# Performance work log

Measured on AMD Instinct MI355X. Metric: run time of the kernel, lower is better.

## Reference

```python
import jax, jax.numpy as jnp
import numpy as np

N_NODES = 100000
E_ORIG = 600000   # entries in edge_dict_original -> nodes of second stage
E_LINE = 1200000  # edges among edge-nodes
H = 128
OUT = 64
BN_EPS = 1e-5
N_LAYERS = 2  # num_initial_gin_layers == num_gin_layers == 2


def setup_inputs() -> dict:
    key = jax.random.key(0)
    ks = iter(jax.random.split(key, 64))
    def nrm(shape, s=0.05):
        return jax.random.normal(next(ks), shape, jnp.float32) * s
    inp = {}
    inp["edge_index"] = jax.random.randint(next(ks), (2, E_LINE), 0, E_ORIG)
    inp["x_original"] = jax.random.normal(next(ks), (N_NODES, H), jnp.float32)
    inp["edge_index_original"] = jax.random.randint(next(ks), (2, E_ORIG), 0, N_NODES)
    inp["edge_pairs"] = jax.random.randint(next(ks), (E_ORIG, 2), 0, N_NODES)
    for pfx in ("init", "gin"):
        inp[pfx + "_W1"] = nrm((N_LAYERS, H, H))
        inp[pfx + "_b1"] = nrm((N_LAYERS, H))
        inp[pfx + "_g"] = jnp.ones((N_LAYERS, H), jnp.float32) + nrm((N_LAYERS, H))
        inp[pfx + "_bb"] = nrm((N_LAYERS, H))
        inp[pfx + "_m"] = nrm((N_LAYERS, H))
        inp[pfx + "_v"] = jnp.ones((N_LAYERS, H), jnp.float32) + jax.random.uniform(next(ks), (N_LAYERS, H), jnp.float32) * 0.1
        inp[pfx + "_W2"] = nrm((N_LAYERS, H, H))
        inp[pfx + "_b2"] = nrm((N_LAYERS, H))
    inp["mlp_W1"] = nrm((H, H)); inp["mlp_b1"] = nrm((H,))
    inp["mlp_g"] = jnp.ones((H,), jnp.float32) + nrm((H,))
    inp["mlp_bb"] = nrm((H,)); inp["mlp_m"] = nrm((H,))
    inp["mlp_v"] = jnp.ones((H,), jnp.float32) + jax.random.uniform(next(ks), (H,), jnp.float32) * 0.1
    inp["mlp_W2"] = nrm((H, H)); inp["mlp_b2"] = nrm((H,))
    inp["out_W"] = nrm((H, OUT)); inp["out_b"] = nrm((OUT,))
    return inp


def _bn(h, g, b, m, v):  # eval-mode BatchNorm1d
    return (h - m) * jax.lax.rsqrt(v + BN_EPS) * g + b


def _gin_conv(x, ei, n, W1, b1, g, bb, m, v, W2, b2):
    # GINConv (eps=0): nn(x + sum_{j in N(i)} x_j)
    agg = jax.ops.segment_sum(x[ei[0]], ei[1], num_segments=n)
    h = x + agg
    h = jax.nn.relu(_bn(h @ W1 + b1, g, bb, m, v))
    return jax.nn.relu(h @ W2 + b2)


def reference(edge_index, x_original, edge_index_original, edge_pairs,
              init_W1, init_b1, init_g, init_bb, init_m, init_v, init_W2, init_b2,
              mlp_W1, mlp_b1, mlp_g, mlp_bb, mlp_m, mlp_v, mlp_W2, mlp_b2,
              gin_W1, gin_b1, gin_g, gin_bb, gin_m, gin_v, gin_W2, gin_b2,
              out_W, out_b):
    x = x_original
    for i in range(N_LAYERS):  # initial GIN layers on original graph (dropout=eval identity)
        x = _gin_conv(x, edge_index_original, N_NODES,
                      init_W1[i], init_b1[i], init_g[i], init_bb[i], init_m[i], init_v[i],
                      init_W2[i], init_b2[i])
    # per-edge gather of node pairs; concat-then-split == two gathers
    def mlp(h):  # PyG MLP, 2 layers, plain last
        h = jax.nn.relu(_bn(h @ mlp_W1 + mlp_b1, mlp_g, mlp_bb, mlp_m, mlp_v))
        return h @ mlp_W2 + mlp_b2
    h = mlp(x[edge_pairs[:, 0]]) + mlp(x[edge_pairs[:, 1]])  # [E_ORIG, H]
    for i in range(N_LAYERS):  # GIN layers on edge-node graph
        h = _gin_conv(h, edge_index, E_ORIG,
                      gin_W1[i], gin_b1[i], gin_g[i], gin_bb[i], gin_m[i], gin_v[i],
                      gin_W2[i], gin_b2[i])
    return h @ out_W + out_b  # [E_ORIG, OUT]
```

## Files before the change

### kernel.cpp

```cpp
#include <hip/hip_runtime.h>
#include <hip/hip_bf16.h>

typedef __bf16 bf8_t __attribute__((ext_vector_type(8)));
typedef float  f32x4 __attribute__((ext_vector_type(4)));

constexpr int N_NODES = 100000;
constexpr int E_ORIG  = 600000;
constexpr int E_LINE  = 1200000;

static inline int cdiv(int a, int b) { return (a + b - 1) / b; }

enum { A_DENSE = 0, A_AGG = 1, A_PAIR = 2 };

__global__ void k_f2b(const float* __restrict__ X, __bf16* __restrict__ O, int n8) {
    int i = blockIdx.x * 256 + threadIdx.x;
    if (i >= n8) return;
    float4 a = ((const float4*)X)[2 * i], b = ((const float4*)X)[2 * i + 1];
    bf8_t o;
    o[0] = (__bf16)a.x; o[1] = (__bf16)a.y; o[2] = (__bf16)a.z; o[3] = (__bf16)a.w;
    o[4] = (__bf16)b.x; o[5] = (__bf16)b.y; o[6] = (__bf16)b.z; o[7] = (__bf16)b.w;
    ((bf8_t*)O)[i] = o;
}

__global__ void k_hist(const int* __restrict__ dst, int* __restrict__ cnt, int E) {
    int e = blockIdx.x * 256 + threadIdx.x;
    if (e < E) atomicAdd(&cnt[dst[e]], 1);
}

__global__ void k_scan1(const int* __restrict__ cnt, int* __restrict__ offs,
                        int* __restrict__ bsum, int n) {
    __shared__ int tmp[256];
    int i = blockIdx.x * 256 + threadIdx.x;
    int v = (i < n) ? cnt[i] : 0;
    tmp[threadIdx.x] = v; __syncthreads();
    #pragma unroll
    for (int d = 1; d < 256; d <<= 1) {
        int t = (threadIdx.x >= d) ? tmp[threadIdx.x - d] : 0;
        __syncthreads();
        tmp[threadIdx.x] += t;
        __syncthreads();
    }
    if (i < n) offs[i] = tmp[threadIdx.x] - v;
    if (threadIdx.x == 255) bsum[blockIdx.x] = tmp[255];
}

__global__ void k_scan2(int* __restrict__ bsum, int nb) {
    __shared__ int tmp[256];
    __shared__ int carry;
    if (threadIdx.x == 0) carry = 0;
    __syncthreads();
    for (int base = 0; base < nb; base += 256) {
        int i = base + threadIdx.x;
        int v = (i < nb) ? bsum[i] : 0;
        tmp[threadIdx.x] = v; __syncthreads();
        #pragma unroll
        for (int d = 1; d < 256; d <<= 1) {
            int t = (threadIdx.x >= d) ? tmp[threadIdx.x - d] : 0;
            __syncthreads();
            tmp[threadIdx.x] += t;
            __syncthreads();
        }
        int tot = tmp[255];
        if (i < nb) bsum[i] = tmp[threadIdx.x] - v + carry;
        __syncthreads();
        if (threadIdx.x == 0) carry += tot;
        __syncthreads();
    }
}

__global__ void k_scan3(int* __restrict__ offs, int* __restrict__ cur,
                        const int* __restrict__ bsum, int n) {
    int i = blockIdx.x * 256 + threadIdx.x;
    if (i >= n) return;
    int o = offs[i] + bsum[blockIdx.x];
    offs[i] = o;
    cur[i]  = o;
}

__global__ void k_fill(const int* __restrict__ src, const int* __restrict__ dst,
                       int* __restrict__ cur, int* __restrict__ adj, int E) {
    int e = blockIdx.x * 256 + threadIdx.x;
    if (e >= E) return;
    int p = atomicAdd(&cur[dst[e]], 1);
    adj[p] = src[e];
}

struct WPtrs { const float* p[10]; };

__global__ void k_packW(WPtrs wp, __bf16* __restrict__ out) {
    const float* W = wp.p[blockIdx.x];
    __bf16* O = out + (size_t)blockIdx.x * 16384;
    const float4* W4 = (const float4*)W;
    for (int e = threadIdx.x; e < 4096; e += 256) {
        float4 w = W4[e];
        unsigned flat = (unsigned)e * 4;
        unsigned k = flat >> 7, n = flat & 127;
        unsigned c = n >> 4, s = k >> 5, hi = (k >> 3) & 3, j = k & 7;
        unsigned l0 = (hi << 4) | (n & 15);
        unsigned base = ((c * 4 + s) * 64 + l0) * 8 + j;
        O[base]      = (__bf16)w.x;
        O[base + 8]  = (__bf16)w.y;
        O[base + 16] = (__bf16)w.z;
        O[base + 24] = (__bf16)w.w;
    }
}

template<int MODE, bool RELU2>
__launch_bounds__(256, 4)
__global__ void k_layer(const __bf16* __restrict__ X, int M,
                        const int* __restrict__ offs, const int* __restrict__ cnt,
                        const int* __restrict__ adj, const int* __restrict__ pairs,
                        const __bf16* __restrict__ Wp1, const __bf16* __restrict__ Wp2,
                        const float* __restrict__ b1,
                        const float* __restrict__ bg, const float* __restrict__ bb,
                        const float* __restrict__ bm, const float* __restrict__ bv,
                        const float* __restrict__ b2,
                        __bf16* __restrict__ out) {
    __shared__ __bf16 sA[128 * 128];

    const int tid  = threadIdx.x;
    const int lane = tid & 63;
    const int wv   = tid >> 6;
    const int rowBase = blockIdx.x * 128;
    const int m0 = lane & 15, kq = lane >> 4;

    if (MODE != A_DENSE) {
        const int c    = lane & 15;
        const int slot = lane >> 4;
        int sarr[8], narr[8];
        #pragma unroll
        for (int p = 0; p < 8; ++p) {
            int grow = rowBase + wv * 32 + p * 4 + slot;
            int g = grow < M ? grow : 0;
            sarr[p] = offs[g];
            narr[p] = grow < M ? cnt[g] : 0;
        }
        int pa0[8], pa1[8];
        #pragma unroll
        for (int p = 0; p < 8; ++p) {
            pa0[p] = narr[p] > 0 ? adj[sarr[p]]     : 0;
            pa1[p] = narr[p] > 1 ? adj[sarr[p] + 1] : 0;
        }

        if (MODE == A_AGG) {
            #pragma unroll
            for (int half = 0; half < 2; ++half) {
                bf8_t sv[4], n0[4], n1[4];
                #pragma unroll
                for (int q = 0; q < 4; ++q) {
                    int p = half * 4 + q;
                    int grow = rowBase + wv * 32 + p * 4 + slot;
                    int g = grow < M ? grow : 0;
                    sv[q] = *((const bf8_t*)(X + (size_t)g      * 128) + c);
                    n0[q] = *((const bf8_t*)(X + (size_t)pa0[p] * 128) + c);
                    n1[q] = *((const bf8_t*)(X + (size_t)pa1[p] * 128) + c);
                }
                #pragma unroll
                for (int q = 0; q < 4; ++q) {
                    int p = half * 4 + q;
                    int rl = wv * 32 + p * 4 + slot;
                    int n = narr[p];
                    float acc[8];
                    #pragma unroll
                    for (int j = 0; j < 8; ++j) {
                        float a = (float)sv[q][j];
                        if (n > 0) a += (float)n0[q][j];
                        if (n > 1) a += (float)n1[q][j];
                        acc[j] = a;
                    }
                    int s = sarr[p], k = 2;
                    for (; k + 2 <= n; k += 2) {
                        int a0 = adj[s + k], a1 = adj[s + k + 1];
                        bf8_t v0 = *((const bf8_t*)(X + (size_t)a0 * 128) + c);
                        bf8_t v1 = *((const bf8_t*)(X + (size_t)a1 * 128) + c);
                        #pragma unroll
                        for (int j = 0; j < 8; ++j) acc[j] += (float)v0[j] + (float)v1[j];
                    }
                    if (k < n) {
                        int a0 = adj[s + k];
                        bf8_t v0 = *((const bf8_t*)(X + (size_t)a0 * 128) + c);
                        #pragma unroll
                        for (int j = 0; j < 8; ++j) acc[j] += (float)v0[j];
                    }
                    bf8_t o;
                    #pragma unroll
                    for (int j = 0; j < 8; ++j) o[j] = (__bf16)acc[j];
                    *(bf8_t*)&sA[rl * 128 + ((c ^ (rl & 7)) << 3)] = o;
                }
            }
        } else {
            #pragma unroll
            for (int half = 0; half < 2; ++half) {
                int2 spr[4], pq0[4], pq1[4];
                #pragma unroll
                for (int q = 0; q < 4; ++q) {
                    int p = half * 4 + q;
                    int grow = rowBase + wv * 32 + p * 4 + slot;
                    int g = grow < M ? grow : 0;
                    spr[q] = ((const int2*)pairs)[g];
                    pq0[q] = ((const int2*)pairs)[pa0[p]];
                    pq1[q] = ((const int2*)pairs)[pa1[p]];
                }
                #pragma unroll
                for (int q = 0; q < 4; ++q) {
                    int p = half * 4 + q;
                    int rl = wv * 32 + p * 4 + slot;
                    int n = narr[p];
                    bf8_t s0 = *((const bf8_t*)(X + (size_t)spr[q].x * 128) + c);
                    bf8_t s1 = *((const bf8_t*)(X + (size_t)spr[q].y * 128) + c);
                    bf8_t u0 = *((const bf8_t*)(X + (size_t)pq0[q].x * 128) + c);
                    bf8_t u1 = *((const bf8_t*)(X + (size_t)pq0[q].y * 128) + c);
                    bf8_t u2 = *((const bf8_t*)(X + (size_t)pq1[q].x * 128) + c);
                    bf8_t u3 = *((const bf8_t*)(X + (size_t)pq1[q].y * 128) + c);
                    float acc[8];
                    #pragma unroll
                    for (int j = 0; j < 8; ++j) {
                        float a = (float)s0[j] + (float)s1[j];
                        if (n > 0) a += (float)u0[j] + (float)u1[j];
                        if (n > 1) a += (float)u2[j] + (float)u3[j];
                        acc[j] = a;
                    }
                    int s = sarr[p];
                    for (int k = 2; k < n; ++k) {
                        int a0 = adj[s + k];
                        int2 qq = ((const int2*)pairs)[a0];
                        bf8_t w0 = *((const bf8_t*)(X + (size_t)qq.x * 128) + c);
                        bf8_t w1 = *((const bf8_t*)(X + (size_t)qq.y * 128) + c);
                        #pragma unroll
                        for (int j = 0; j < 8; ++j) acc[j] += (float)w0[j] + (float)w1[j];
                    }
                    bf8_t o;
                    #pragma unroll
                    for (int j = 0; j < 8; ++j) o[j] = (__bf16)acc[j];
                    *(bf8_t*)&sA[rl * 128 + ((c ^ (rl & 7)) << 3)] = o;
                }
            }
        }
    }

    f32x4 acc[2][8];
    #pragma unroll
    for (int rt = 0; rt < 2; ++rt)
        #pragma unroll
        for (int ct = 0; ct < 8; ++ct) acc[rt][ct] = (f32x4){0.f, 0.f, 0.f, 0.f};

    #pragma unroll
    for (int s = 0; s < 4; ++s) {
        bf8_t fa[2];
        #pragma unroll
        for (int rt = 0; rt < 2; ++rt) {
            int rl = wv * 32 + rt * 16 + m0;
            if (MODE == A_DENSE) {
                int r = rowBase + rl;
                r = r < M ? r : M - 1;
                fa[rt] = *(const bf8_t*)(X + (size_t)r * 128 + s * 32 + kq * 8);
            } else {
                int chunk = s * 4 + kq;
                fa[rt] = *(const bf8_t*)&sA[rl * 128 + ((chunk ^ (rl & 7)) << 3)];
            }
        }
        #pragma unroll
        for (int ct = 0; ct < 8; ++ct) {
            bf8_t fw = *(const bf8_t*)(Wp1 + ((size_t)((ct * 4 + s) * 64 + lane)) * 8);
            #pragma unroll
            for (int rt = 0; rt < 2; ++rt)
                acc[rt][ct] = __builtin_amdgcn_mfma_f32_16x16x32_bf16(fa[rt], fw, acc[rt][ct], 0, 0, 0);
        }
    }

    float S1r[8], T1r[8], T2r[8];
    #pragma unroll
    for (int ct = 0; ct < 8; ++ct) {
        int col = ct * 16 + m0;
        float b = b1[col];
        float g = bg[col], be = bb[col], m_ = bm[col], v_ = bv[col];
        float S = g * rsqrtf(v_ + 1e-5f);
        S1r[ct] = S;
        T1r[ct] = b * S + (be - m_ * S);
        T2r[ct] = b2[col];
    }

    #pragma unroll
    for (int rt = 0; rt < 2; ++rt) {
        #pragma unroll
        for (int r = 0; r < 4; ++r) {
            int rl = wv * 32 + rt * 16 + kq * 4 + r;
            #pragma unroll
            for (int ct = 0; ct < 8; ++ct) {
                int col = ct * 16 + m0;
                float v = acc[rt][ct][r] * S1r[ct] + T1r[ct];
                v = fmaxf(v, 0.f);
                int chunk = col >> 3;
                sA[rl * 128 + ((chunk ^ (rl & 7)) << 3) + (col & 7)] = (__bf16)v;
            }
        }
    }

    f32x4 acc2[2][8];
    #pragma unroll
    for (int rt = 0; rt < 2; ++rt)
        #pragma unroll
        for (int ct = 0; ct < 8; ++ct) acc2[rt][ct] = (f32x4){0.f, 0.f, 0.f, 0.f};

    #pragma unroll
    for (int s = 0; s < 4; ++s) {
        bf8_t fa[2];
        #pragma unroll
        for (int rt = 0; rt < 2; ++rt) {
            int rl = wv * 32 + rt * 16 + m0;
            int chunk = s * 4 + kq;
            fa[rt] = *(const bf8_t*)&sA[rl * 128 + ((chunk ^ (rl & 7)) << 3)];
        }
        #pragma unroll
        for (int ct = 0; ct < 8; ++ct) {
            bf8_t fw = *(const bf8_t*)(Wp2 + ((size_t)((ct * 4 + s) * 64 + lane)) * 8);
            #pragma unroll
            for (int rt = 0; rt < 2; ++rt)
                acc2[rt][ct] = __builtin_amdgcn_mfma_f32_16x16x32_bf16(fa[rt], fw, acc2[rt][ct], 0, 0, 0);
        }
    }

    #pragma unroll
    for (int rt = 0; rt < 2; ++rt) {
        #pragma unroll
        for (int r = 0; r < 4; ++r) {
            int row = rowBase + wv * 32 + rt * 16 + kq * 4 + r;
            if (row < M) {
                #pragma unroll
                for (int ct = 0; ct < 8; ++ct) {
                    int col = ct * 16 + m0;
                    float v = acc2[rt][ct][r] + T2r[ct];
                    if (RELU2) v = fmaxf(v, 0.f);
                    out[(size_t)row * 128 + col] = (__bf16)v;
                }
            }
        }
    }
}

template<int NC, bool BN, bool RELU, bool OUTF32>
__launch_bounds__(256, 2)
__global__ void k_gemm(const __bf16* __restrict__ A, int M,
                       const float* __restrict__ W,
                       const float* __restrict__ bias,
                       const float* __restrict__ bg, const float* __restrict__ bb,
                       const float* __restrict__ bm, const float* __restrict__ bv,
                       void* __restrict__ outp) {
    constexpr int NT = NC / 16;
    __shared__ __bf16 sW[128 * NC];
    __shared__ float sS[NC];
    __shared__ float sT[NC];

    const float4* W4 = (const float4*)W;
    for (int e = threadIdx.x; e < 32 * NC; e += 256) {
        float4 w = W4[e];
        unsigned flat = (unsigned)e * 4;
        unsigned k = flat / NC, n = flat % NC;
        unsigned c = n >> 4, s = k >> 5, hi = (k >> 3) & 3, j = k & 7;
        unsigned l0 = (hi << 4) | (n & 15);
        unsigned base = ((c * 4 + s) * 64 + l0) * 8 + j;
        sW[base]      = (__bf16)w.x;
        sW[base + 8]  = (__bf16)w.y;
        sW[base + 16] = (__bf16)w.z;
        sW[base + 24] = (__bf16)w.w;
    }
    for (int n = threadIdx.x; n < NC; n += 256) {
        float b = bias[n];
        float S = 1.0f, T = b;
        if (BN) {
            float g = bg[n], be = bb[n], m = bm[n], v = bv[n];
            S = g * rsqrtf(v + 1e-5f);
            T = b * S + (be - m * S);
        }
        sS[n] = S; sT[n] = T;
    }
    __syncthreads();

    const int lane = threadIdx.x & 63;
    const int wv   = threadIdx.x >> 6;
    const int rowBase = blockIdx.x * 256 + wv * 64;
    const int m0 = lane & 15, kq = lane >> 4;

    f32x4 acc[4][NT];
    #pragma unroll
    for (int rt = 0; rt < 4; ++rt)
        #pragma unroll
        for (int ct = 0; ct < NT; ++ct)
            acc[rt][ct] = (f32x4){0.f, 0.f, 0.f, 0.f};

    #pragma unroll
    for (int s = 0; s < 4; ++s) {
        bf8_t fa[4];
        #pragma unroll
        for (int rt = 0; rt < 4; ++rt) {
            int r = rowBase + rt * 16 + m0;
            r = r < M ? r : M - 1;
            fa[rt] = *(const bf8_t*)(A + (size_t)r * 128 + s * 32 + kq * 8);
        }
        #pragma unroll
        for (int ct = 0; ct < NT; ++ct) {
            bf8_t fw = *(const bf8_t*)&sW[((ct * 4 + s) * 64 + lane) * 8];
            #pragma unroll
            for (int rt = 0; rt < 4; ++rt)
                acc[rt][ct] = __builtin_amdgcn_mfma_f32_16x16x32_bf16(fa[rt], fw, acc[rt][ct], 0, 0, 0);
        }
    }

    #pragma unroll
    for (int rt = 0; rt < 4; ++rt) {
        #pragma unroll
        for (int r = 0; r < 4; ++r) {
            int row = rowBase + rt * 16 + kq * 4 + r;
            if (row < M) {
                #pragma unroll
                for (int ct = 0; ct < NT; ++ct) {
                    int col = ct * 16 + m0;
                    float v = acc[rt][ct][r] * sS[col] + sT[col];
                    if (RELU) v = fmaxf(v, 0.0f);
                    size_t o = (size_t)row * NC + col;
                    if constexpr (OUTF32) ((float*)outp)[o]  = v;
                    else                  ((__bf16*)outp)[o] = (__bf16)v;
                }
            }
        }
    }
}

extern "C" void kernel_launch(void* const* d_in, const int* in_sizes, int n_in,
                              void* d_out, int out_size, void* d_ws, size_t ws_size,
                              hipStream_t stream) {
    const int*   edge_index = (const int*)d_in[0];
    const float* x_orig     = (const float*)d_in[1];
    const int*   eio        = (const int*)d_in[2];
    const int*   pairs      = (const int*)d_in[3];
    const float* iW1 = (const float*)d_in[4];
    const float* ib1 = (const float*)d_in[5];
    const float* ig  = (const float*)d_in[6];
    const float* ibb = (const float*)d_in[7];
    const float* im  = (const float*)d_in[8];
    const float* iv  = (const float*)d_in[9];
    const float* iW2 = (const float*)d_in[10];
    const float* ib2 = (const float*)d_in[11];
    const float* gW1 = (const float*)d_in[12];
    const float* gb1 = (const float*)d_in[13];
    const float* gg  = (const float*)d_in[14];
    const float* gbb = (const float*)d_in[15];
    const float* gm  = (const float*)d_in[16];
    const float* gv  = (const float*)d_in[17];
    const float* gW2 = (const float*)d_in[18];
    const float* gb2 = (const float*)d_in[19];
    const float* mW1 = (const float*)d_in[20];
    const float* mb1 = (const float*)d_in[21];
    const float* mg  = (const float*)d_in[22];
    const float* mbb = (const float*)d_in[23];
    const float* mm  = (const float*)d_in[24];
    const float* mv  = (const float*)d_in[25];
    const float* mW2 = (const float*)d_in[26];
    const float* mb2 = (const float*)d_in[27];
    const float* oW  = (const float*)d_in[28];
    const float* ob  = (const float*)d_in[29];

    char* w = (char*)d_ws;
    __bf16* EB  = (__bf16*)w;                w += (size_t)E_ORIG * 128 * 2;
    __bf16* XB  = (__bf16*)w;                w += (size_t)N_NODES * 128 * 2;
    __bf16* NA  = (__bf16*)w;                w += (size_t)N_NODES * 128 * 2;
    __bf16* NB  = (__bf16*)w;                w += (size_t)N_NODES * 128 * 2;
    int* cnt  = (int*)w;                     w += (size_t)E_ORIG * 4;
    int* offs = (int*)w;                     w += (size_t)E_ORIG * 4;
    int* cur  = (int*)w;                     w += (size_t)E_ORIG * 4;
    int* bsum = (int*)w;                     w += 4096 * 4;
    int* adj  = (int*)w;                     w += (size_t)E_LINE * 4;
    __bf16* Wpk = (__bf16*)w;
    __bf16* EBd = (__bf16*)d_out;

    const int* eio_src = eio;
    const int* eio_dst = eio + E_ORIG;
    const int* el_src  = edge_index;
    const int* el_dst  = edge_index + E_LINE;

    const int nBlk = cdiv(N_NODES, 128);
    const int eBlk = cdiv(E_ORIG, 128);
    const int nScanNB = cdiv(N_NODES, 256);
    const int eScanNB = cdiv(E_ORIG, 256);

    WPtrs wp;
    wp.p[0] = iW1;          wp.p[1] = iW2;
    wp.p[2] = iW1 + 16384;  wp.p[3] = iW2 + 16384;
    wp.p[4] = mW1;          wp.p[5] = mW2;
    wp.p[6] = gW1;          wp.p[7] = gW2;
    wp.p[8] = gW1 + 16384;  wp.p[9] = gW2 + 16384;
    k_packW<<<10, 256, 0, stream>>>(wp, Wpk);

    hipMemsetAsync(cnt, 0, (size_t)N_NODES * 4, stream);
    k_hist <<<cdiv(E_ORIG, 256), 256, 0, stream>>>(eio_dst, cnt, E_ORIG);
    k_scan1<<<nScanNB, 256, 0, stream>>>(cnt, offs, bsum, N_NODES);
    k_scan2<<<1, 256, 0, stream>>>(bsum, nScanNB);
    k_scan3<<<nScanNB, 256, 0, stream>>>(offs, cur, bsum, N_NODES);
    k_fill <<<cdiv(E_ORIG, 256), 256, 0, stream>>>(eio_src, eio_dst, cur, adj, E_ORIG);

    k_f2b<<<cdiv(N_NODES * 16, 256), 256, 0, stream>>>(x_orig, XB, N_NODES * 16);
    k_layer<A_AGG, true><<<nBlk, 256, 0, stream>>>(XB, N_NODES, offs, cnt, adj, nullptr,
        Wpk + 0 * 16384, Wpk + 1 * 16384, ib1, ig, ibb, im, iv, ib2, NA);
    k_layer<A_AGG, true><<<nBlk, 256, 0, stream>>>(NA, N_NODES, offs, cnt, adj, nullptr,
        Wpk + 2 * 16384, Wpk + 3 * 16384, ib1 + 128, ig + 128, ibb + 128, im + 128, iv + 128, ib2 + 128, NB);
    k_layer<A_DENSE, false><<<nBlk, 256, 0, stream>>>(NB, N_NODES, nullptr, nullptr, nullptr, nullptr,
        Wpk + 4 * 16384, Wpk + 5 * 16384, mb1, mg, mbb, mm, mv, mb2, XB);

    hipMemsetAsync(cnt, 0, (size_t)E_ORIG * 4, stream);
    k_hist <<<cdiv(E_LINE, 256), 256, 0, stream>>>(el_dst, cnt, E_LINE);
    k_scan1<<<eScanNB, 256, 0, stream>>>(cnt, offs, bsum, E_ORIG);
    k_scan2<<<1, 256, 0, stream>>>(bsum, eScanNB);
    k_scan3<<<eScanNB, 256, 0, stream>>>(offs, cur, bsum, E_ORIG);
    k_fill <<<cdiv(E_LINE, 256), 256, 0, stream>>>(el_src, el_dst, cur, adj, E_LINE);

    k_layer<A_PAIR, true><<<eBlk, 256, 0, stream>>>(XB, E_ORIG, offs, cnt, adj, pairs,
        Wpk + 6 * 16384, Wpk + 7 * 16384, gb1, gg, gbb, gm, gv, gb2, EBd);
    k_layer<A_AGG, true><<<eBlk, 256, 0, stream>>>(EBd, E_ORIG, offs, cnt, adj, nullptr,
        Wpk + 8 * 16384, Wpk + 9 * 16384, gb1 + 128, gg + 128, gbb + 128, gm + 128, gv + 128, gb2 + 128, EB);

    k_gemm<64, false, false, true><<<cdiv(E_ORIG, 256), 256, 0, stream>>>(EB, E_ORIG, oW, ob,
        nullptr, nullptr, nullptr, nullptr, d_out);
}
```

Measured before the change: 1.082 ms.

## Fuse MLP and output projection into GIN layer kernels, shrink blocks to 64 rows

Chains extra GEMM stages inside the per-layer kernel through shared memory. The node MLP now runs inside the second initial GIN layer, and the output projection inside the last edge GIN layer, which removes two standalone kernels and their intermediate global round trips. Blocks shrink to 128 threads and 64 rows with a smaller LDS tile. Gather loads are also reordered so all neighbour loads are issued before accumulation. The cost is longer kernels with more register pressure and a different occupancy profile.

```diff
diff --git a/kernel.cpp b/kernel.cpp
--- a/kernel.cpp
+++ b/kernel.cpp
@@ -10,7 +10,7 @@
 
 static inline int cdiv(int a, int b) { return (a + b - 1) / b; }
 
-enum { A_DENSE = 0, A_AGG = 1, A_PAIR = 2 };
+enum { A_AGG = 1, A_PAIR = 2 };
 
 __global__ void k_f2b(const float* __restrict__ X, __bf16* __restrict__ O, int n8) {
     int i = blockIdx.x * 256 + threadIdx.x;
@@ -85,16 +85,18 @@
     adj[p] = src[e];
 }
 
-struct WPtrs { const float* p[10]; };
+struct WPtrs { const float* p[11]; int nc[11]; };
 
 __global__ void k_packW(WPtrs wp, __bf16* __restrict__ out) {
     const float* W = wp.p[blockIdx.x];
+    const int NC = wp.nc[blockIdx.x];
     __bf16* O = out + (size_t)blockIdx.x * 16384;
     const float4* W4 = (const float4*)W;
-    for (int e = threadIdx.x; e < 4096; e += 256) {
+    const int tot = 32 * NC;
+    for (int e = threadIdx.x; e < tot; e += 256) {
         float4 w = W4[e];
         unsigned flat = (unsigned)e * 4;
-        unsigned k = flat >> 7, n = flat & 127;
+        unsigned k = flat / NC, n = flat % NC;
         unsigned c = n >> 4, s = k >> 5, hi = (k >> 3) & 3, j = k & 7;
         unsigned l0 = (hi << 4) | (n & 15);
         unsigned base = ((c * 4 + s) * 64 + l0) * 8 + j;
@@ -105,32 +107,125 @@
     }
 }
 
-template<int MODE, bool RELU2>
-__launch_bounds__(256, 4)
+
+template<int NT>
+__device__ __forceinline__ void mm_from_lds(const __bf16* sA, const __bf16* __restrict__ Wp,
+                                            int wv, int lane, f32x4 (&acc)[2][NT]) {
+    const int m0 = lane & 15, kq = lane >> 4;
+    #pragma unroll
+    for (int s = 0; s < 4; ++s) {
+        bf8_t fa[2];
+        #pragma unroll
+        for (int rt = 0; rt < 2; ++rt) {
+            int rl = wv * 32 + rt * 16 + m0;
+            int chunk = s * 4 + kq;
+            fa[rt] = *(const bf8_t*)&sA[rl * 128 + ((chunk ^ (rl & 7)) << 3)];
+        }
+        #pragma unroll
+        for (int ct = 0; ct < NT; ++ct) {
+            bf8_t fw = *(const bf8_t*)(Wp + ((size_t)((ct * 4 + s) * 64 + lane)) * 8);
+            #pragma unroll
+            for (int rt = 0; rt < 2; ++rt)
+                acc[rt][ct] = __builtin_amdgcn_mfma_f32_16x16x32_bf16(fa[rt], fw, acc[rt][ct], 0, 0, 0);
+        }
+    }
+}
+
+template<int NT>
+__device__ __forceinline__ void zero_acc(f32x4 (&acc)[2][NT]) {
+    #pragma unroll
+    for (int rt = 0; rt < 2; ++rt)
+        #pragma unroll
+        for (int ct = 0; ct < NT; ++ct) acc[rt][ct] = (f32x4){0.f, 0.f, 0.f, 0.f};
+}
+
+template<bool BN_>
+__device__ __forceinline__ void epi_to_lds(__bf16* sA, int wv, int lane, f32x4 (&acc)[2][8],
+        const float* __restrict__ b, const float* __restrict__ g,
+        const float* __restrict__ bb, const float* __restrict__ m,
+        const float* __restrict__ v) {
+    const int m0 = lane & 15, kq = lane >> 4;
+    float S[8], T[8];
+    #pragma unroll
+    for (int ct = 0; ct < 8; ++ct) {
+        int col = ct * 16 + m0;
+        float bias = b[col];
+        if (BN_) {
+            float gg = g[col], be = bb[col], mm_ = m[col], vv = v[col];
+            float s_ = gg * rsqrtf(vv + 1e-5f);
+            S[ct] = s_; T[ct] = bias * s_ + (be - mm_ * s_);
+        } else { S[ct] = 1.f; T[ct] = bias; }
+    }
+    #pragma unroll
+    for (int rt = 0; rt < 2; ++rt)
+        #pragma unroll
+        for (int r = 0; r < 4; ++r) {
+            int rl = wv * 32 + rt * 16 + kq * 4 + r;
+            #pragma unroll
+            for (int ct = 0; ct < 8; ++ct) {
+                int col = ct * 16 + m0;
+                float val = acc[rt][ct][r] * S[ct] + T[ct];
+                val = fmaxf(val, 0.f);
+                sA[rl * 128 + (((col >> 3) ^ (rl & 7)) << 3) + (col & 7)] = (__bf16)val;
+            }
+        }
+}
+
+template<int NT, bool RELU_, bool F32OUT>
+__device__ __forceinline__ void epi_to_global(int wv, int lane, int rowBase, int M,
+        f32x4 (&acc)[2][NT], const float* __restrict__ bias, void* outp) {
+    const int m0 = lane & 15, kq = lane >> 4;
+    float T[NT];
+    #pragma unroll
+    for (int ct = 0; ct < NT; ++ct) T[ct] = bias[ct * 16 + m0];
+    #pragma unroll
+    for (int rt = 0; rt < 2; ++rt)
+        #pragma unroll
+        for (int r = 0; r < 4; ++r) {
+            int row = rowBase + wv * 32 + rt * 16 + kq * 4 + r;
+            if (row < M) {
+                #pragma unroll
+                for (int ct = 0; ct < NT; ++ct) {
+                    int col = ct * 16 + m0;
+                    float val = acc[rt][ct][r] + T[ct];
+                    if (RELU_) val = fmaxf(val, 0.f);
+                    if (F32OUT) ((float*)outp)[(size_t)row * (NT * 16) + col] = val;
+                    else        ((__bf16*)outp)[(size_t)row * (NT * 16) + col] = (__bf16)val;
+                }
+            }
+        }
+}
+
+struct LP {
+    const float *b0, *g0, *bb0, *m0, *v0;
+    const float *b1;
+    const float *b2, *g2, *bb2, *m2, *v2;
+    const float *b3;
+};
+
+template<int MODE, int NSTAGES>
+__launch_bounds__(128, 4)
 __global__ void k_layer(const __bf16* __restrict__ X, int M,
                         const int* __restrict__ offs, const int* __restrict__ cnt,
                         const int* __restrict__ adj, const int* __restrict__ pairs,
-                        const __bf16* __restrict__ Wp1, const __bf16* __restrict__ Wp2,
-                        const float* __restrict__ b1,
-                        const float* __restrict__ bg, const float* __restrict__ bb,
-                        const float* __restrict__ bm, const float* __restrict__ bv,
-                        const float* __restrict__ b2,
-                        __bf16* __restrict__ out) {
-    __shared__ __bf16 sA[128 * 128];
+                        const __bf16* __restrict__ W0, const __bf16* __restrict__ W1,
+                        const __bf16* __restrict__ W2, const __bf16* __restrict__ W3,
+                        LP lp, void* __restrict__ outp) {
+    __shared__ __bf16 sA[64 * 128];
 
     const int tid  = threadIdx.x;
     const int lane = tid & 63;
     const int wv   = tid >> 6;
-    const int rowBase = blockIdx.x * 128;
-    const int m0 = lane & 15, kq = lane >> 4;
-
-    if (MODE != A_DENSE) {
+    const int rowBase = blockIdx.x * 64;
+
+    {
         const int c    = lane & 15;
         const int slot = lane >> 4;
+        const int rb   = rowBase + wv * 32;
         int sarr[8], narr[8];
         #pragma unroll
         for (int p = 0; p < 8; ++p) {
-            int grow = rowBase + wv * 32 + p * 4 + slot;
+            int grow = rb + p * 4 + slot;
             int g = grow < M ? grow : 0;
             sarr[p] = offs[g];
             narr[p] = grow < M ? cnt[g] : 0;
@@ -143,82 +238,89 @@
         }
 
         if (MODE == A_AGG) {
-            #pragma unroll
-            for (int half = 0; half < 2; ++half) {
-                bf8_t sv[4], n0[4], n1[4];
-                #pragma unroll
-                for (int q = 0; q < 4; ++q) {
-                    int p = half * 4 + q;
-                    int grow = rowBase + wv * 32 + p * 4 + slot;
-                    int g = grow < M ? grow : 0;
-                    sv[q] = *((const bf8_t*)(X + (size_t)g      * 128) + c);
-                    n0[q] = *((const bf8_t*)(X + (size_t)pa0[p] * 128) + c);
-                    n1[q] = *((const bf8_t*)(X + (size_t)pa1[p] * 128) + c);
-                }
-                #pragma unroll
-                for (int q = 0; q < 4; ++q) {
-                    int p = half * 4 + q;
-                    int rl = wv * 32 + p * 4 + slot;
-                    int n = narr[p];
-                    float acc[8];
+            bf8_t sv[8], n0[8], n1[8];
+            #pragma unroll
+            for (int p = 0; p < 8; ++p) {
+                int grow = rb + p * 4 + slot;
+                int g = grow < M ? grow : 0;
+                sv[p] = *((const bf8_t*)(X + (size_t)g * 128) + c);
+            }
+            #pragma unroll
+            for (int p = 0; p < 8; ++p) n0[p] = *((const bf8_t*)(X + (size_t)pa0[p] * 128) + c);
+            #pragma unroll
+            for (int p = 0; p < 8; ++p) n1[p] = *((const bf8_t*)(X + (size_t)pa1[p] * 128) + c);
+            #pragma unroll
+            for (int p = 0; p < 8; ++p) {
+                int rl = wv * 32 + p * 4 + slot;
+                int n = narr[p];
+                float a[8];
+                #pragma unroll
+                for (int j = 0; j < 8; ++j) {
+                    float t = (float)sv[p][j];
+                    if (n > 0) t += (float)n0[p][j];
+                    if (n > 1) t += (float)n1[p][j];
+                    a[j] = t;
+                }
+                int s = sarr[p], k = 2;
+                for (; k + 2 <= n; k += 2) {
+                    int a0 = adj[s + k], a1 = adj[s + k + 1];
+                    bf8_t v0 = *((const bf8_t*)(X + (size_t)a0 * 128) + c);
+                    bf8_t v1 = *((const bf8_t*)(X + (size_t)a1 * 128) + c);
                     #pragma unroll
-                    for (int j = 0; j < 8; ++j) {
-                        float a = (float)sv[q][j];
-                        if (n > 0) a += (float)n0[q][j];
-                        if (n > 1) a += (float)n1[q][j];
-                        acc[j] = a;
-                    }
-                    int s = sarr[p], k = 2;
-                    for (; k + 2 <= n; k += 2) {
-                        int a0 = adj[s + k], a1 = adj[s + k + 1];
-                        bf8_t v0 = *((const bf8_t*)(X + (size_t)a0 * 128) + c);
-                        bf8_t v1 = *((const bf8_t*)(X + (size_t)a1 * 128) + c);
-                        #pragma unroll
-                        for (int j = 0; j < 8; ++j) acc[j] += (float)v0[j] + (float)v1[j];
-                    }
-                    if (k < n) {
-                        int a0 = adj[s + k];
-                        bf8_t v0 = *((const bf8_t*)(X + (size_t)a0 * 128) + c);
-                        #pragma unroll
-                        for (int j = 0; j < 8; ++j) acc[j] += (float)v0[j];
-                    }
-                    bf8_t o;
+                    for (int j = 0; j < 8; ++j) a[j] += (float)v0[j] + (float)v1[j];
+                }
+                if (k < n) {
+                    int a0 = adj[s + k];
+                    bf8_t v0 = *((const bf8_t*)(X + (size_t)a0 * 128) + c);
                     #pragma unroll
-                    for (int j = 0; j < 8; ++j) o[j] = (__bf16)acc[j];
-                    *(bf8_t*)&sA[rl * 128 + ((c ^ (rl & 7)) << 3)] = o;
-                }
+                    for (int j = 0; j < 8; ++j) a[j] += (float)v0[j];
+                }
+                bf8_t o;
+                #pragma unroll
+                for (int j = 0; j < 8; ++j) o[j] = (__bf16)a[j];
+                *(bf8_t*)&sA[rl * 128 + ((c ^ (rl & 7)) << 3)] = o;
             }
         } else {
             #pragma unroll
-            for (int half = 0; half < 2; ++half) {
+            for (int hp = 0; hp < 2; ++hp) {
                 int2 spr[4], pq0[4], pq1[4];
                 #pragma unroll
                 for (int q = 0; q < 4; ++q) {
-                    int p = half * 4 + q;
-                    int grow = rowBase + wv * 32 + p * 4 + slot;
+                    int p = hp * 4 + q;
+                    int grow = rb + p * 4 + slot;
                     int g = grow < M ? grow : 0;
                     spr[q] = ((const int2*)pairs)[g];
                     pq0[q] = ((const int2*)pairs)[pa0[p]];
                     pq1[q] = ((const int2*)pairs)[pa1[p]];
                 }
+                bf8_t s0[4], s1[4], u0[4], u1[4], u2[4], u3[4];
                 #pragma unroll
                 for (int q = 0; q < 4; ++q) {
-                    int p = half * 4 + q;
+                    s0[q] = *((const bf8_t*)(X + (size_t)spr[q].x * 128) + c);
+                    s1[q] = *((const bf8_t*)(X + (size_t)spr[q].y * 128) + c);
+                }
+                #pragma unroll
+                for (int q = 0; q < 4; ++q) {
+                    u0[q] = *((const bf8_t*)(X + (size_t)pq0[q].x * 128) + c);
+                    u1[q] = *((const bf8_t*)(X + (size_t)pq0[q].y * 128) + c);
+                }
+                #pragma unroll
+                for (int q = 0; q < 4; ++q) {
+                    u2[q] = *((const bf8_t*)(X + (size_t)pq1[q].x * 128) + c);
+                    u3[q] = *((const bf8_t*)(X + (size_t)pq1[q].y * 128) + c);
+                }
+                #pragma unroll
+                for (int q = 0; q < 4; ++q) {
+                    int p = hp * 4 + q;
                     int rl = wv * 32 + p * 4 + slot;
                     int n = narr[p];
-                    bf8_t s0 = *((const bf8_t*)(X + (size_t)spr[q].x * 128) + c);
-                    bf8_t s1 = *((const bf8_t*)(X + (size_t)spr[q].y * 128) + c);
-                    bf8_t u0 = *((const bf8_t*)(X + (size_t)pq0[q].x * 128) + c);
-                    bf8_t u1 = *((const bf8_t*)(X + (size_t)pq0[q].y * 128) + c);
-                    bf8_t u2 = *((const bf8_t*)(X + (size_t)pq1[q].x * 128) + c);
-                    bf8_t u3 = *((const bf8_t*)(X + (size_t)pq1[q].y * 128) + c);
-                    float acc[8];
+                    float a[8];
                     #pragma unroll
                     for (int j = 0; j < 8; ++j) {
-                        float a = (float)s0[j] + (float)s1[j];
-                        if (n > 0) a += (float)u0[j] + (float)u1[j];
-                        if (n > 1) a += (float)u2[j] + (float)u3[j];
-                        acc[j] = a;
+                        float t = (float)s0[q][j] + (float)s1[q][j];
+                        if (n > 0) t += (float)u0[q][j] + (float)u1[q][j];
+                        if (n > 1) t += (float)u2[q][j] + (float)u3[q][j];
+                        a[j] = t;
                     }
                     int s = sarr[p];
                     for (int k = 2; k < n; ++k) {
@@ -227,11 +329,11 @@
                         bf8_t w0 = *((const bf8_t*)(X + (size_t)qq.x * 128) + c);
                         bf8_t w1 = *((const bf8_t*)(X + (size_t)qq.y * 128) + c);
                         #pragma unroll
-                        for (int j = 0; j < 8; ++j) acc[j] += (float)w0[j] + (float)w1[j];
+                        for (int j = 0; j < 8; ++j) a[j] += (float)w0[j] + (float)w1[j];
                     }
                     bf8_t o;
                     #pragma unroll
-                    for (int j = 0; j < 8; ++j) o[j] = (__bf16)acc[j];
+                    for (int j = 0; j < 8; ++j) o[j] = (__bf16)a[j];
                     *(bf8_t*)&sA[rl * 128 + ((c ^ (rl & 7)) << 3)] = o;
                 }
             }
@@ -239,189 +341,28 @@
     }
 
     f32x4 acc[2][8];
-    #pragma unroll
-    for (int rt = 0; rt < 2; ++rt)
-        #pragma unroll
-        for (int ct = 0; ct < 8; ++ct) acc[rt][ct] = (f32x4){0.f, 0.f, 0.f, 0.f};
-
-    #pragma unroll
-    for (int s = 0; s < 4; ++s) {
-        bf8_t fa[2];
-        #pragma unroll
-        for (int rt = 0; rt < 2; ++rt) {
-            int rl = wv * 32 + rt * 16 + m0;
-            if (MODE == A_DENSE) {
-                int r = rowBase + rl;
-                r = r < M ? r : M - 1;
-                fa[rt] = *(const bf8_t*)(X + (size_t)r * 128 + s * 32 + kq * 8);
-            } else {
-                int chunk = s * 4 + kq;
-                fa[rt] = *(const bf8_t*)&sA[rl * 128 + ((chunk ^ (rl & 7)) << 3)];
-            }
-        }
-        #pragma unroll
-        for (int ct = 0; ct < 8; ++ct) {
-            bf8_t fw = *(const bf8_t*)(Wp1 + ((size_t)((ct * 4 + s) * 64 + lane)) * 8);
-            #pragma unroll
-            for (int rt = 0; rt < 2; ++rt)
-                acc[rt][ct] = __builtin_amdgcn_mfma_f32_16x16x32_bf16(fa[rt], fw, acc[rt][ct], 0, 0, 0);
-        }
-    }
-
-    float S1r[8], T1r[8], T2r[8];
-    #pragma unroll
-    for (int ct = 0; ct < 8; ++ct) {
-        int col = ct * 16 + m0;
-        float b = b1[col];
-        float g = bg[col], be = bb[col], m_ = bm[col], v_ = bv[col];
-        float S = g * rsqrtf(v_ + 1e-5f);
-        S1r[ct] = S;
-        T1r[ct] = b * S + (be - m_ * S);
-        T2r[ct] = b2[col];
-    }
-
-    #pragma unroll
-    for (int rt = 0; rt < 2; ++rt) {
-        #pragma unroll
-        for (int r = 0; r < 4; ++r) {
-            int rl = wv * 32 + rt * 16 + kq * 4 + r;
-            #pragma unroll
-            for (int ct = 0; ct < 8; ++ct) {
-                int col = ct * 16 + m0;
-                float v = acc[rt][ct][r] * S1r[ct] + T1r[ct];
-                v = fmaxf(v, 0.f);
-                int chunk = col >> 3;
-                sA[rl * 128 + ((chunk ^ (rl & 7)) << 3) + (col & 7)] = (__bf16)v;
-            }
-        }
-    }
-
-    f32x4 acc2[2][8];
-    #pragma unroll
-    for (int rt = 0; rt < 2; ++rt)
-        #pragma unroll
-        for (int ct = 0; ct < 8; ++ct) acc2[rt][ct] = (f32x4){0.f, 0.f, 0.f, 0.f};
-
-    #pragma unroll
-    for (int s = 0; s < 4; ++s) {
-        bf8_t fa[2];
-        #pragma unroll
-        for (int rt = 0; rt < 2; ++rt) {
-            int rl = wv * 32 + rt * 16 + m0;
-            int chunk = s * 4 + kq;
-            fa[rt] = *(const bf8_t*)&sA[rl * 128 + ((chunk ^ (rl & 7)) << 3)];
-        }
-        #pragma unroll
-        for (int ct = 0; ct < 8; ++ct) {
-            bf8_t fw = *(const bf8_t*)(Wp2 + ((size_t)((ct * 4 + s) * 64 + lane)) * 8);
-            #pragma unroll
-            for (int rt = 0; rt < 2; ++rt)
-                acc2[rt][ct] = __builtin_amdgcn_mfma_f32_16x16x32_bf16(fa[rt], fw, acc2[rt][ct], 0, 0, 0);
-        }
-    }
-
-    #pragma unroll
-    for (int rt = 0; rt < 2; ++rt) {
-        #pragma unroll
-        for (int r = 0; r < 4; ++r) {
-            int row = rowBase + wv * 32 + rt * 16 + kq * 4 + r;
-            if (row < M) {
-                #pragma unroll
-                for (int ct = 0; ct < 8; ++ct) {
-                    int col = ct * 16 + m0;
-                    float v = acc2[rt][ct][r] + T2r[ct];
-                    if (RELU2) v = fmaxf(v, 0.f);
-                    out[(size_t)row * 128 + col] = (__bf16)v;
-                }
-            }
-        }
-    }
-}
-
-template<int NC, bool BN, bool RELU, bool OUTF32>
-__launch_bounds__(256, 2)
-__global__ void k_gemm(const __bf16* __restrict__ A, int M,
-                       const float* __restrict__ W,
-                       const float* __restrict__ bias,
-                       const float* __restrict__ bg, const float* __restrict__ bb,
-                       const float* __restrict__ bm, const float* __restrict__ bv,
-                       void* __restrict__ outp) {
-    constexpr int NT = NC / 16;
-    __shared__ __bf16 sW[128 * NC];
-    __shared__ float sS[NC];
-    __shared__ float sT[NC];
-
-    const float4* W4 = (const float4*)W;
-    for (int e = threadIdx.x; e < 32 * NC; e += 256) {
-        float4 w = W4[e];
-        unsigned flat = (unsigned)e * 4;
-        unsigned k = flat / NC, n = flat % NC;
-        unsigned c = n >> 4, s = k >> 5, hi = (k >> 3) & 3, j = k & 7;
-        unsigned l0 = (hi << 4) | (n & 15);
-        unsigned base = ((c * 4 + s) * 64 + l0) * 8 + j;
-        sW[base]      = (__bf16)w.x;
-        sW[base + 8]  = (__bf16)w.y;
-        sW[base + 16] = (__bf16)w.z;
-        sW[base + 24] = (__bf16)w.w;
-    }
-    for (int n = threadIdx.x; n < NC; n += 256) {
-        float b = bias[n];
-        float S = 1.0f, T = b;
-        if (BN) {
-            float g = bg[n], be = bb[n], m = bm[n], v = bv[n];
-            S = g * rsqrtf(v + 1e-5f);
-            T = b * S + (be - m * S);
-        }
-        sS[n] = S; sT[n] = T;
-    }
-    __syncthreads();
-
-    const int lane = threadIdx.x & 63;
-    const int wv   = threadIdx.x >> 6;
-    const int rowBase = blockIdx.x * 256 + wv * 64;
-    const int m0 = lane & 15, kq = lane >> 4;
-
-    f32x4 acc[4][NT];
-    #pragma unroll
-    for (int rt = 0; rt < 4; ++rt)
-        #pragma unroll
-        for (int ct = 0; ct < NT; ++ct)
-            acc[rt][ct] = (f32x4){0.f, 0.f, 0.f, 0.f};
-
-    #pragma unroll
-    for (int s = 0; s < 4; ++s) {
-        bf8_t fa[4];
-        #pragma unroll
-        for (int rt = 0; rt < 4; ++rt) {
-            int r = rowBase + rt * 16 + m0;
-            r = r < M ? r : M - 1;
-            fa[rt] = *(const bf8_t*)(A + (size_t)r * 128 + s * 32 + kq * 8);
-        }
-        #pragma unroll
-        for (int ct = 0; ct < NT; ++ct) {
-            bf8_t fw = *(const bf8_t*)&sW[((ct * 4 + s) * 64 + lane) * 8];
-            #pragma unroll
-            for (int rt = 0; rt < 4; ++rt)
-                acc[rt][ct] = __builtin_amdgcn_mfma_f32_16x16x32_bf16(fa[rt], fw, acc[rt][ct], 0, 0, 0);
-        }
-    }
-
-    #pragma unroll
-    for (int rt = 0; rt < 4; ++rt) {
-        #pragma unroll
-        for (int r = 0; r < 4; ++r) {
-            int row = rowBase + rt * 16 + kq * 4 + r;
-            if (row < M) {
-                #pragma unroll
-                for (int ct = 0; ct < NT; ++ct) {
-                    int col = ct * 16 + m0;
-                    float v = acc[rt][ct][r] * sS[col] + sT[col];
-                    if (RELU) v = fmaxf(v, 0.0f);
-                    size_t o = (size_t)row * NC + col;
-                    if constexpr (OUTF32) ((float*)outp)[o]  = v;
-                    else                  ((__bf16*)outp)[o] = (__bf16)v;
-                }
-            }
+    zero_acc<8>(acc);
+    mm_from_lds<8>(sA, W0, wv, lane, acc);
+    epi_to_lds<true>(sA, wv, lane, acc, lp.b0, lp.g0, lp.bb0, lp.m0, lp.v0);
+
+    zero_acc<8>(acc);
+    mm_from_lds<8>(sA, W1, wv, lane, acc);
+    if constexpr (NSTAGES == 2) {
+        epi_to_global<8, true, false>(wv, lane, rowBase, M, acc, lp.b1, outp);
+    } else {
+        epi_to_lds<false>(sA, wv, lane, acc, lp.b1, nullptr, nullptr, nullptr, nullptr);
+        if constexpr (NSTAGES == 4) {
+            zero_acc<8>(acc);
+            mm_from_lds<8>(sA, W2, wv, lane, acc);
+            epi_to_lds<true>(sA, wv, lane, acc, lp.b2, lp.g2, lp.bb2, lp.m2, lp.v2);
+            zero_acc<8>(acc);
+            mm_from_lds<8>(sA, W3, wv, lane, acc);
+            epi_to_global<8, false, false>(wv, lane, rowBase, M, acc, lp.b3, outp);
+        } else {
+            f32x4 acc3[2][4];
+            zero_acc<4>(acc3);
+            mm_from_lds<4>(sA, W2, wv, lane, acc3);
+            epi_to_global<4, false, true>(wv, lane, rowBase, M, acc3, lp.b2, outp);
         }
     }
 }
@@ -464,32 +405,36 @@
     __bf16* EB  = (__bf16*)w;                w += (size_t)E_ORIG * 128 * 2;
     __bf16* XB  = (__bf16*)w;                w += (size_t)N_NODES * 128 * 2;
     __bf16* NA  = (__bf16*)w;                w += (size_t)N_NODES * 128 * 2;
-    __bf16* NB  = (__bf16*)w;                w += (size_t)N_NODES * 128 * 2;
     int* cnt  = (int*)w;                     w += (size_t)E_ORIG * 4;
     int* offs = (int*)w;                     w += (size_t)E_ORIG * 4;
     int* cur  = (int*)w;                     w += (size_t)E_ORIG * 4;
     int* bsum = (int*)w;                     w += 4096 * 4;
     int* adj  = (int*)w;                     w += (size_t)E_LINE * 4;
     __bf16* Wpk = (__bf16*)w;
-    __bf16* EBd = (__bf16*)d_out;
 
     const int* eio_src = eio;
     const int* eio_dst = eio + E_ORIG;
     const int* el_src  = edge_index;
     const int* el_dst  = edge_index + E_LINE;
 
-    const int nBlk = cdiv(N_NODES, 128);
-    const int eBlk = cdiv(E_ORIG, 128);
+    const int nBlk = cdiv(N_NODES, 64);
+    const int eBlk = cdiv(E_ORIG, 64);
     const int nScanNB = cdiv(N_NODES, 256);
     const int eScanNB = cdiv(E_ORIG, 256);
 
     WPtrs wp;
-    wp.p[0] = iW1;          wp.p[1] = iW2;
-    wp.p[2] = iW1 + 16384;  wp.p[3] = iW2 + 16384;
-    wp.p[4] = mW1;          wp.p[5] = mW2;
-    wp.p[6] = gW1;          wp.p[7] = gW2;
-    wp.p[8] = gW1 + 16384;  wp.p[9] = gW2 + 16384;
-    k_packW<<<10, 256, 0, stream>>>(wp, Wpk);
+    wp.p[0] = iW1;          wp.nc[0] = 128;
+    wp.p[1] = iW2;          wp.nc[1] = 128;
+    wp.p[2] = iW1 + 16384;  wp.nc[2] = 128;
+    wp.p[3] = iW2 + 16384;  wp.nc[3] = 128;
+    wp.p[4] = mW1;          wp.nc[4] = 128;
+    wp.p[5] = mW2;          wp.nc[5] = 128;
+    wp.p[6] = gW1;          wp.nc[6] = 128;
+    wp.p[7] = gW2;          wp.nc[7] = 128;
+    wp.p[8] = gW1 + 16384;  wp.nc[8] = 128;
+    wp.p[9] = gW2 + 16384;  wp.nc[9] = 128;
+    wp.p[10] = oW;          wp.nc[10] = 64;
+    k_packW<<<11, 256, 0, stream>>>(wp, Wpk);
 
     hipMemsetAsync(cnt, 0, (size_t)N_NODES * 4, stream);
     k_hist <<<cdiv(E_ORIG, 256), 256, 0, stream>>>(eio_dst, cnt, E_ORIG);
@@ -499,12 +444,20 @@
     k_fill <<<cdiv(E_ORIG, 256), 256, 0, stream>>>(eio_src, eio_dst, cur, adj, E_ORIG);
 
     k_f2b<<<cdiv(N_NODES * 16, 256), 256, 0, stream>>>(x_orig, XB, N_NODES * 16);
-    k_layer<A_AGG, true><<<nBlk, 256, 0, stream>>>(XB, N_NODES, offs, cnt, adj, nullptr,
-        Wpk + 0 * 16384, Wpk + 1 * 16384, ib1, ig, ibb, im, iv, ib2, NA);
-    k_layer<A_AGG, true><<<nBlk, 256, 0, stream>>>(NA, N_NODES, offs, cnt, adj, nullptr,
-        Wpk + 2 * 16384, Wpk + 3 * 16384, ib1 + 128, ig + 128, ibb + 128, im + 128, iv + 128, ib2 + 128, NB);
-    k_layer<A_DENSE, false><<<nBlk, 256, 0, stream>>>(NB, N_NODES, nullptr, nullptr, nullptr, nullptr,
-        Wpk + 4 * 16384, Wpk + 5 * 16384, mb1, mg, mbb, mm, mv, mb2, XB);
+
+    LP lp0{};
+    lp0.b0 = ib1;  lp0.g0 = ig;  lp0.bb0 = ibb;  lp0.m0 = im;  lp0.v0 = iv;
+    lp0.b1 = ib2;
+    k_layer<A_AGG, 2><<<nBlk, 128, 0, stream>>>(XB, N_NODES, offs, cnt, adj, nullptr,
+        Wpk + 0 * 16384, Wpk + 1 * 16384, nullptr, nullptr, lp0, NA);
+
+    LP lp1{};
+    lp1.b0 = ib1 + 128; lp1.g0 = ig + 128; lp1.bb0 = ibb + 128; lp1.m0 = im + 128; lp1.v0 = iv + 128;
+    lp1.b1 = ib2 + 128;
+    lp1.b2 = mb1; lp1.g2 = mg; lp1.bb2 = mbb; lp1.m2 = mm; lp1.v2 = mv;
+    lp1.b3 = mb2;
+    k_layer<A_AGG, 4><<<nBlk, 128, 0, stream>>>(NA, N_NODES, offs, cnt, adj, nullptr,
+        Wpk + 2 * 16384, Wpk + 3 * 16384, Wpk + 4 * 16384, Wpk + 5 * 16384, lp1, XB);
 
     hipMemsetAsync(cnt, 0, (size_t)E_ORIG * 4, stream);
     k_hist <<<cdiv(E_LINE, 256), 256, 0, stream>>>(el_dst, cnt, E_LINE);
@@ -513,11 +466,16 @@
     k_scan3<<<eScanNB, 256, 0, stream>>>(offs, cur, bsum, E_ORIG);
     k_fill <<<cdiv(E_LINE, 256), 256, 0, stream>>>(el_src, el_dst, cur, adj, E_LINE);
 
-    k_layer<A_PAIR, true><<<eBlk, 256, 0, stream>>>(XB, E_ORIG, offs, cnt, adj, pairs,
-        Wpk + 6 * 16384, Wpk + 7 * 16384, gb1, gg, gbb, gm, gv, gb2, EBd);
-    k_layer<A_AGG, true><<<eBlk, 256, 0, stream>>>(EBd, E_ORIG, offs, cnt, adj, nullptr,
-        Wpk + 8 * 16384, Wpk + 9 * 16384, gb1 + 128, gg + 128, gbb + 128, gm + 128, gv + 128, gb2 + 128, EB);
-
-    k_gemm<64, false, false, true><<<cdiv(E_ORIG, 256), 256, 0, stream>>>(EB, E_ORIG, oW, ob,
-        nullptr, nullptr, nullptr, nullptr, d_out);
-}
+    LP lp2{};
+    lp2.b0 = gb1;  lp2.g0 = gg;  lp2.bb0 = gbb;  lp2.m0 = gm;  lp2.v0 = gv;
+    lp2.b1 = gb2;
+    k_layer<A_PAIR, 2><<<eBlk, 128, 0, stream>>>(XB, E_ORIG, offs, cnt, adj, pairs,
+        Wpk + 6 * 16384, Wpk + 7 * 16384, nullptr, nullptr, lp2, EB);
+
+    LP lp3{};
+    lp3.b0 = gb1 + 128; lp3.g0 = gg + 128; lp3.bb0 = gbb + 128; lp3.m0 = gm + 128; lp3.v0 = gv + 128;
+    lp3.b1 = gb2 + 128;
+    lp3.b2 = ob;
+    k_layer<A_AGG, 3><<<eBlk, 128, 0, stream>>>(EB, E_ORIG, offs, cnt, adj, nullptr,
+        Wpk + 8 * 16384, Wpk + 9 * 16384, Wpk + 10 * 16384, nullptr, lp3, d_out);
+}
```

Measured after the change: 1.225 ms. 1.13x slower.
